# Optimization experiments

Measured on AMD Instinct MI355X. Metric: run time of the kernel, lower is better.

The kernel has to match this reference:

```python
import jax, jax.numpy as jnp
import numpy as np

NUM_HEADS = 16

def setup_inputs() -> dict:
    key = jax.random.key(0)
    ks = jax.random.split(key, 5)
    b, c, w, h = 2, 1024, 48, 48
    sc = 0.02
    return {
        "x": jax.random.normal(ks[0], (b, c, w, h), jnp.float32),
        "Wqkv": jax.random.normal(ks[1], (3 * c, c), jnp.float32) * sc,
        "bqkv": jax.random.normal(ks[2], (3 * c,), jnp.float32) * sc,
        "Wo": jax.random.normal(ks[3], (c, c), jnp.float32) * sc,
        "bo": jax.random.normal(ks[4], (c,), jnp.float32) * sc,
    }

def reference(x, Wqkv, bqkv, Wo, bo):
    b, c, w, h = x.shape
    n = NUM_HEADS
    hd = c // n
    s = w * h
    # [b,c,w,h] -> tokens [b, s, c]
    xs = x.transpose(0, 2, 3, 1).reshape(b, s, c)
    qkv = xs @ Wqkv.T + bqkv                       # [b, s, 3c]
    # rearrange 'b s (three n hd) -> three b n s hd'
    qkv = qkv.reshape(b, s, 3, n, hd).transpose(2, 0, 3, 1, 4)
    q, k, v = qkv[0], qkv[1], qkv[2]               # [b, n, s, hd]
    score = jnp.einsum('bnqh,bnkh->bnqk', q, k) / jnp.sqrt(jnp.float32(hd))
    # module uses a soft causal mask: subtract 10000 above the diagonal
    mask = 10000.0 * jnp.triu(jnp.ones((s, s), dtype=score.dtype), k=1)
    attn = jax.nn.softmax(score - mask, axis=-1)   # [b, n, s, s]
    z = jnp.einsum('bnqk,bnkh->bqnh', attn, v).reshape(b, s, c)
    out = z @ Wo.T + bo                            # [b, s, c]
    return out.reshape(b, w, h, c).transpose(0, 3, 1, 2)
```

## Files before the change

### kernel.cpp

```cpp
#include <hip/hip_runtime.h>

typedef __bf16 bf16;
typedef __bf16 bf16x8 __attribute__((ext_vector_type(8)));
typedef float floatx4 __attribute__((ext_vector_type(4)));

static constexpr int S = 2304;
static constexpr int C = 1024;
static constexpr int NHEAD = 16;
static constexpr int HDIM = 64;
static constexpr int BATCH = 2;

__global__ __launch_bounds__(256) void k_convert(const float* __restrict__ src,
                                                 bf16* __restrict__ dst, int n8) {
  int i = blockIdx.x * 256 + threadIdx.x;
  if (i >= n8) return;
  float4 a = *(const float4*)(src + (size_t)i * 8);
  float4 b = *(const float4*)(src + (size_t)i * 8 + 4);
  bf16x8 o;
  o[0] = (bf16)a.x; o[1] = (bf16)a.y; o[2] = (bf16)a.z; o[3] = (bf16)a.w;
  o[4] = (bf16)b.x; o[5] = (bf16)b.y; o[6] = (bf16)b.z; o[7] = (bf16)b.w;
  *(bf16x8*)(dst + (size_t)i * 8) = o;
}

__global__ __launch_bounds__(256) void k_transpose(const float* __restrict__ x,
                                                   bf16* __restrict__ xs) {
  __shared__ bf16 T[64 * 72];
  int c0 = blockIdx.x * 64, t0 = blockIdx.y * 64, b = blockIdx.z;
  int tid = threadIdx.x;
  const float* xb = x + (size_t)b * C * S;
#pragma unroll
  for (int it = 0; it < 4; ++it) {
    int idx = it * 256 + tid;
    int rc = idx >> 4, t4 = idx & 15;
    float4 v = *(const float4*)(xb + (size_t)(c0 + rc) * S + t0 + t4 * 4);
    T[(t4 * 4 + 0) * 72 + rc] = (bf16)v.x;
    T[(t4 * 4 + 1) * 72 + rc] = (bf16)v.y;
    T[(t4 * 4 + 2) * 72 + rc] = (bf16)v.z;
    T[(t4 * 4 + 3) * 72 + rc] = (bf16)v.w;
  }
  __syncthreads();
  bf16* xsb = xs + (size_t)b * S * C;
#pragma unroll
  for (int it = 0; it < 2; ++it) {
    int idx = it * 256 + tid;
    int rt = idx >> 3, c8 = idx & 7;
    bf16x8 v;
#pragma unroll
    for (int i = 0; i < 8; ++i) v[i] = T[rt * 72 + c8 * 8 + i];
    *(bf16x8*)(xsb + (size_t)(t0 + rt) * C + c0 + c8 * 8) = v;
  }
}

__device__ __forceinline__ void g2l16(const bf16* g, bf16* l) {
  __builtin_amdgcn_global_load_lds(
      (const __attribute__((address_space(1))) void*)g,
      (__attribute__((address_space(3))) void*)l, 16, 0, 0);
}

template <int EPI>
__global__ __launch_bounds__(256) void k_gemm_bt(const bf16* __restrict__ A,
                                                 const bf16* __restrict__ Bt,
                                                 const float* __restrict__ bias,
                                                 bf16* __restrict__ q,
                                                 bf16* __restrict__ k,
                                                 bf16* __restrict__ v,
                                                 float* __restrict__ outf) {
  constexpr int K = C;
  __shared__ bf16 As[128 * 32];
  __shared__ bf16 Bs[128 * 32];
  int tid = threadIdx.x;
  int w = tid >> 6, lane = tid & 63, ln = lane & 15, quad = lane >> 4;
  int m0 = blockIdx.y * 128, n0 = blockIdx.x * 128;
  int moff = (w >> 1) * 64, noff = (w & 1) * 64;
  floatx4 acc[4][4] = {};

  for (int k0 = 0; k0 < K; k0 += 32) {
    __syncthreads();
#pragma unroll
    for (int it = 0; it < 2; ++it) {
      int cb = (it * 4 + w) * 64;
      int g = cb + lane;
      int row = g >> 2, c4 = g & 3;
      g2l16(A + (size_t)(m0 + row) * K + k0 + c4 * 8, As + cb * 8);
      g2l16(Bt + (size_t)(n0 + row) * K + k0 + c4 * 8, Bs + cb * 8);
    }
    __syncthreads();
    bf16x8 af[4], bfr[4];
#pragma unroll
    for (int i = 0; i < 4; ++i) {
      af[i]  = *(const bf16x8*)(As + (moff + i * 16 + ln) * 32 + quad * 8);
      bfr[i] = *(const bf16x8*)(Bs + (noff + i * 16 + ln) * 32 + quad * 8);
    }
#pragma unroll
    for (int im = 0; im < 4; ++im)
#pragma unroll
      for (int in = 0; in < 4; ++in)
        acc[im][in] = __builtin_amdgcn_mfma_f32_16x16x32_bf16(
            af[im], bfr[in], acc[im][in], 0, 0, 0);
  }

  int bidx = (m0 >= S) ? 1 : 0;
  if (EPI == 0) {
#pragma unroll
    for (int in = 0; in < 4; ++in) {
      int j = n0 + noff + in * 16 + ln;
      float bv = bias[j];
      int three = j >> 10;
      int head = (j >> 6) & 15;
      int hdi = j & 63;
#pragma unroll
      for (int im = 0; im < 4; ++im) {
        int mbase = m0 + moff + im * 16 + quad * 4;
        int tb = mbase - bidx * S;
        if (three == 2) {
          union { ushort4 u; bf16 h[4]; } P;
#pragma unroll
          for (int r = 0; r < 4; ++r) P.h[r] = (bf16)(acc[im][in][r] + bv);
          *(ushort4*)(v + ((size_t)(bidx * NHEAD + head) * HDIM + hdi) * S + tb) = P.u;
        } else {
          bf16* dst = (three == 0 ? q : k) +
                      ((size_t)(bidx * NHEAD + head) * S + tb) * HDIM + hdi;
#pragma unroll
          for (int r = 0; r < 4; ++r) dst[(size_t)r * HDIM] = (bf16)(acc[im][in][r] + bv);
        }
      }
    }
  } else {
#pragma unroll
    for (int in = 0; in < 4; ++in) {
      int co = n0 + noff + in * 16 + ln;
      float bv = bias[co];
#pragma unroll
      for (int im = 0; im < 4; ++im) {
        int mbase = m0 + moff + im * 16 + quad * 4;
        int tb = mbase - bidx * S;
        float4 st;
        st.x = acc[im][in][0] + bv;
        st.y = acc[im][in][1] + bv;
        st.z = acc[im][in][2] + bv;
        st.w = acc[im][in][3] + bv;
        *(float4*)(outf + ((size_t)bidx * C + co) * S + tb) = st;
      }
    }
  }
}

__global__ __launch_bounds__(256) void k_attn(const bf16* __restrict__ Qg,
                                              const bf16* __restrict__ Kg,
                                              const bf16* __restrict__ Vtg,
                                              bf16* __restrict__ z) {
  __shared__ bf16 Ks[2][64 * 64];
  __shared__ bf16 Vs[2][64 * 64];
  __shared__ bf16 Pt[64 * 72];
  int i = blockIdx.x;
  int xcd = i & 7, j = i >> 3;
  int grp = j / 36, jq = j % 36;
  int qi = 35 - jq;
  int bh = xcd + 8 * grp;
  int b = bh >> 4, h = bh & 15;
  int tid = threadIdx.x;
  int w = tid >> 6, lane = tid & 63, ln = lane & 15, quad = lane >> 4;
  int q0 = qi * 64;
  int qg = q0 + w * 16 + ln;

  const bf16* kb = Kg + (size_t)bh * S * HDIM;
  const bf16* vb = Vtg + (size_t)bh * HDIM * S;

  int s_row = tid >> 3, s_c8 = tid & 7;
  int s_cs = s_c8 ^ (s_row & 7);
  int s_row2 = (256 + tid) >> 3;
  int s_cs2 = s_c8 ^ (s_row2 & 7);

  const bf16* qb = Qg + ((size_t)bh * S + qg) * HDIM + quad * 8;
  bf16x8 qf0 = *(const bf16x8*)qb;
  bf16x8 qf1 = *(const bf16x8*)(qb + 32);

  float lsum = 0.f;
  floatx4 o_acc[4] = {};

  {
    g2l16(kb + (size_t)s_row * HDIM + s_cs * 8, Ks[0] + tid * 8);
    g2l16(vb + (size_t)s_row * S + s_cs * 8, Vs[0] + tid * 8);
    g2l16(kb + (size_t)s_row2 * HDIM + s_cs2 * 8, Ks[0] + (256 + tid) * 8);
    g2l16(vb + (size_t)s_row2 * S + s_cs2 * 8, Vs[0] + (256 + tid) * 8);
  }

#pragma unroll 1
  for (int kt = 0; kt <= qi; ++kt) {
    int cur = kt & 1;
    __syncthreads();

    if (kt < qi) {
      int nxt = 1 - cur;
      const bf16* kbn = kb + (size_t)(kt + 1) * 64 * HDIM;
      const bf16* vbn = vb + (size_t)(kt + 1) * 64;
      g2l16(kbn + (size_t)s_row * HDIM + s_cs * 8, Ks[nxt] + tid * 8);
      g2l16(vbn + (size_t)s_row * S + s_cs * 8, Vs[nxt] + tid * 8);
      g2l16(kbn + (size_t)s_row2 * HDIM + s_cs2 * 8, Ks[nxt] + (256 + tid) * 8);
      g2l16(vbn + (size_t)s_row2 * S + s_cs2 * 8, Vs[nxt] + (256 + tid) * 8);
    }

    floatx4 s_acc[4] = {};
#pragma unroll
    for (int kf = 0; kf < 4; ++kf) {
      int row = kf * 16 + ln;
      int sw = row & 7;
      bf16x8 k0 = *(const bf16x8*)(Ks[cur] + row * 64 + ((0 ^ sw) ^ quad) * 8);
      s_acc[kf] = __builtin_amdgcn_mfma_f32_16x16x32_bf16(k0, qf0, s_acc[kf], 0, 0, 0);
      bf16x8 k1 = *(const bf16x8*)(Ks[cur] + row * 64 + ((4 ^ sw) ^ quad) * 8);
      s_acc[kf] = __builtin_amdgcn_mfma_f32_16x16x32_bf16(k1, qf1, s_acc[kf], 0, 0, 0);
    }

#pragma unroll
    for (int kf = 0; kf < 4; ++kf) {
      union { ushort4 u; bf16 hh[4]; } P;
#pragma unroll
      for (int r = 0; r < 4; ++r) {
        int kg = kt * 64 + kf * 16 + quad * 4 + r;
        float pv = (kg > qg) ? 0.f : exp2f(s_acc[kf][r] * 0.180336880f);
        lsum += pv;
        P.hh[r] = (bf16)pv;
      }
      *(ushort4*)(Pt + (w * 16 + ln) * 72 + kf * 16 + quad * 4) = P.u;
    }

#pragma unroll
    for (int t = 0; t < 2; ++t) {
      bf16x8 pf = *(const bf16x8*)(Pt + (w * 16 + ln) * 72 + t * 32 + quad * 8);
#pragma unroll
      for (int hf = 0; hf < 4; ++hf) {
        int row = hf * 16 + ln;
        int sw = row & 7;
        bf16x8 vf = *(const bf16x8*)(Vs[cur] + row * 64 + (((t * 4 + quad) ^ sw)) * 8);
        o_acc[hf] = __builtin_amdgcn_mfma_f32_16x16x32_bf16(vf, pf, o_acc[hf], 0, 0, 0);
      }
    }
  }

  lsum += __shfl_xor(lsum, 16);
  lsum += __shfl_xor(lsum, 32);
  float inv = 1.f / lsum;

  bf16* dst = z + ((size_t)b * S + qg) * C + h * HDIM + quad * 4;
#pragma unroll
  for (int hf = 0; hf < 4; ++hf) {
    union { ushort4 u; bf16 hh[4]; } P;
#pragma unroll
    for (int r = 0; r < 4; ++r) P.hh[r] = (bf16)(o_acc[hf][r] * inv);
    *(ushort4*)(dst + hf * 16) = P.u;
  }
}

extern "C" void kernel_launch(void* const* d_in, const int* in_sizes, int n_in,
                              void* d_out, int out_size, void* d_ws, size_t ws_size,
                              hipStream_t stream) {
  const float* x    = (const float*)d_in[0];
  const float* Wqkv = (const float*)d_in[1];
  const float* bqkv = (const float*)d_in[2];
  const float* Wo   = (const float*)d_in[3];
  const float* bo   = (const float*)d_in[4];
  float* out = (float*)d_out;

  bf16* ws = (bf16*)d_ws;
  const size_t tok = (size_t)BATCH * S * C;
  bf16* xs   = ws;
  bf16* Qg   = ws + tok;
  bf16* Kg   = ws + 2 * tok;
  bf16* Vtg  = ws + 3 * tok;
  bf16* Wqb  = ws + 4 * tok;
  bf16* Wob  = Wqb + (size_t)3 * C * C;
  bf16* z    = xs;

  k_convert<<<(3 * C * C / 8 + 255) / 256, 256, 0, stream>>>(Wqkv, Wqb, 3 * C * C / 8);
  k_convert<<<(C * C / 8 + 255) / 256, 256, 0, stream>>>(Wo, Wob, C * C / 8);
  k_transpose<<<dim3(C / 64, S / 64, BATCH), 256, 0, stream>>>(x, xs);
  k_gemm_bt<0><<<dim3(3 * C / 128, BATCH * S / 128), 256, 0, stream>>>(
      xs, Wqb, bqkv, Qg, Kg, Vtg, nullptr);
  k_attn<<<dim3(1152), 256, 0, stream>>>(Qg, Kg, Vtg, z);
  k_gemm_bt<1><<<dim3(C / 128, BATCH * S / 128), 256, 0, stream>>>(
      z, Wob, bo, nullptr, nullptr, nullptr, out);
}
```

Before: 230.7 us.

## Process 128 queries per attention block and fold softmax scale into Q

The attention kernel now handles two 64-row query tiles per block, so each K/V tile loaded into shared memory is reused by both halves and the grid shrinks from 1152 to 576 blocks. The causal mask test is applied only on diagonal tiles, and the fully masked lower-half tile is skipped. The softmax scale (including the log2e factor) is folded into Q in the QKV GEMM epilogue, which removes a multiply per score. In exchange, register pressure goes up, fewer blocks are available to hide latency, and the causal work is less evenly balanced across blocks.

```diff
diff --git a/kernel.cpp b/kernel.cpp
--- a/kernel.cpp
+++ b/kernel.cpp
@@ -9,6 +9,7 @@
 static constexpr int NHEAD = 16;
 static constexpr int HDIM = 64;
 static constexpr int BATCH = 2;
+static constexpr float QSCALE = 0.18033688011112042f;
 
 __global__ __launch_bounds__(256) void k_convert(const float* __restrict__ src,
                                                  bf16* __restrict__ dst, int n8) {
@@ -117,9 +118,13 @@
 #pragma unroll
           for (int r = 0; r < 4; ++r) P.h[r] = (bf16)(acc[im][in][r] + bv);
           *(ushort4*)(v + ((size_t)(bidx * NHEAD + head) * HDIM + hdi) * S + tb) = P.u;
+        } else if (three == 0) {
+          bf16* dst = q + ((size_t)(bidx * NHEAD + head) * S + tb) * HDIM + hdi;
+#pragma unroll
+          for (int r = 0; r < 4; ++r)
+            dst[(size_t)r * HDIM] = (bf16)((acc[im][in][r] + bv) * QSCALE);
         } else {
-          bf16* dst = (three == 0 ? q : k) +
-                      ((size_t)(bidx * NHEAD + head) * S + tb) * HDIM + hdi;
+          bf16* dst = k + ((size_t)(bidx * NHEAD + head) * S + tb) * HDIM + hdi;
 #pragma unroll
           for (int r = 0; r < 4; ++r) dst[(size_t)r * HDIM] = (bf16)(acc[im][in][r] + bv);
         }
@@ -151,103 +156,183 @@
                                               bf16* __restrict__ z) {
   __shared__ bf16 Ks[2][64 * 64];
   __shared__ bf16 Vs[2][64 * 64];
-  __shared__ bf16 Pt[64 * 72];
+  __shared__ bf16 Pt[128 * 72];
   int i = blockIdx.x;
   int xcd = i & 7, j = i >> 3;
-  int grp = j / 36, jq = j % 36;
-  int qi = 35 - jq;
+  int grp = j / 18, jq = j % 18;
+  int qi = 17 - jq;
   int bh = xcd + 8 * grp;
   int b = bh >> 4, h = bh & 15;
   int tid = threadIdx.x;
   int w = tid >> 6, lane = tid & 63, ln = lane & 15, quad = lane >> 4;
-  int q0 = qi * 64;
-  int qg = q0 + w * 16 + ln;
+  int q0 = qi * 128;
+  int qgL = q0 + w * 16 + ln;
+  int qgU = qgL + 64;
 
   const bf16* kb = Kg + (size_t)bh * S * HDIM;
   const bf16* vb = Vtg + (size_t)bh * HDIM * S;
 
   int s_row = tid >> 3, s_c8 = tid & 7;
   int s_cs = s_c8 ^ (s_row & 7);
-  int s_row2 = (256 + tid) >> 3;
+  int s_row2 = s_row + 32;
   int s_cs2 = s_c8 ^ (s_row2 & 7);
-
-  const bf16* qb = Qg + ((size_t)bh * S + qg) * HDIM + quad * 8;
-  bf16x8 qf0 = *(const bf16x8*)qb;
-  bf16x8 qf1 = *(const bf16x8*)(qb + 32);
-
-  float lsum = 0.f;
-  floatx4 o_acc[4] = {};
-
-  {
-    g2l16(kb + (size_t)s_row * HDIM + s_cs * 8, Ks[0] + tid * 8);
-    g2l16(vb + (size_t)s_row * S + s_cs * 8, Vs[0] + tid * 8);
-    g2l16(kb + (size_t)s_row2 * HDIM + s_cs2 * 8, Ks[0] + (256 + tid) * 8);
-    g2l16(vb + (size_t)s_row2 * S + s_cs2 * 8, Vs[0] + (256 + tid) * 8);
-  }
+  size_t kOff1 = (size_t)s_row * HDIM + s_cs * 8;
+  size_t kOff2 = (size_t)s_row2 * HDIM + s_cs2 * 8;
+  size_t vOff1 = (size_t)s_row * S + s_cs * 8;
+  size_t vOff2 = (size_t)s_row2 * S + s_cs2 * 8;
+
+  const bf16* qbL = Qg + ((size_t)bh * S + qgL) * HDIM + quad * 8;
+  const bf16* qbU = qbL + (size_t)64 * HDIM;
+  bf16x8 qfL0 = *(const bf16x8*)qbL;
+  bf16x8 qfL1 = *(const bf16x8*)(qbL + 32);
+  bf16x8 qfU0 = *(const bf16x8*)qbU;
+  bf16x8 qfU1 = *(const bf16x8*)(qbU + 32);
+
+  float lsumL = 0.f, lsumU = 0.f;
+  floatx4 oL[4] = {}, oU[4] = {};
+
+  int ktMax = 2 * qi + 1;
+
+  g2l16(kb + kOff1, Ks[0] + tid * 8);
+  g2l16(vb + vOff1, Vs[0] + tid * 8);
+  g2l16(kb + kOff2, Ks[0] + (256 + tid) * 8);
+  g2l16(vb + vOff2, Vs[0] + (256 + tid) * 8);
+
+  const bf16* kbn = kb + (size_t)64 * HDIM;
+  const bf16* vbn = vb + 64;
 
 #pragma unroll 1
-  for (int kt = 0; kt <= qi; ++kt) {
+  for (int kt = 0; kt <= ktMax; ++kt) {
     int cur = kt & 1;
     __syncthreads();
 
-    if (kt < qi) {
-      int nxt = 1 - cur;
-      const bf16* kbn = kb + (size_t)(kt + 1) * 64 * HDIM;
-      const bf16* vbn = vb + (size_t)(kt + 1) * 64;
-      g2l16(kbn + (size_t)s_row * HDIM + s_cs * 8, Ks[nxt] + tid * 8);
-      g2l16(vbn + (size_t)s_row * S + s_cs * 8, Vs[nxt] + tid * 8);
-      g2l16(kbn + (size_t)s_row2 * HDIM + s_cs2 * 8, Ks[nxt] + (256 + tid) * 8);
-      g2l16(vbn + (size_t)s_row2 * S + s_cs2 * 8, Vs[nxt] + (256 + tid) * 8);
-    }
-
-    floatx4 s_acc[4] = {};
+    if (kt < ktMax) {
+      bf16* kd = Ks[1 - cur];
+      bf16* vd = Vs[1 - cur];
+      g2l16(kbn + kOff1, kd + tid * 8);
+      g2l16(vbn + vOff1, vd + tid * 8);
+      g2l16(kbn + kOff2, kd + (256 + tid) * 8);
+      g2l16(vbn + vOff2, vd + (256 + tid) * 8);
+      kbn += (size_t)64 * HDIM;
+      vbn += 64;
+    }
+
+    bool maskL = (kt == 2 * qi);
+    bool skipL = (kt == 2 * qi + 1);
+    bool maskU = (kt == 2 * qi + 1);
+
+    floatx4 sL[4] = {}, sU[4] = {};
 #pragma unroll
     for (int kf = 0; kf < 4; ++kf) {
       int row = kf * 16 + ln;
       int sw = row & 7;
-      bf16x8 k0 = *(const bf16x8*)(Ks[cur] + row * 64 + ((0 ^ sw) ^ quad) * 8);
-      s_acc[kf] = __builtin_amdgcn_mfma_f32_16x16x32_bf16(k0, qf0, s_acc[kf], 0, 0, 0);
+      bf16x8 k0 = *(const bf16x8*)(Ks[cur] + row * 64 + (sw ^ quad) * 8);
       bf16x8 k1 = *(const bf16x8*)(Ks[cur] + row * 64 + ((4 ^ sw) ^ quad) * 8);
-      s_acc[kf] = __builtin_amdgcn_mfma_f32_16x16x32_bf16(k1, qf1, s_acc[kf], 0, 0, 0);
-    }
-
-#pragma unroll
-    for (int kf = 0; kf < 4; ++kf) {
-      union { ushort4 u; bf16 hh[4]; } P;
-#pragma unroll
-      for (int r = 0; r < 4; ++r) {
-        int kg = kt * 64 + kf * 16 + quad * 4 + r;
-        float pv = (kg > qg) ? 0.f : exp2f(s_acc[kf][r] * 0.180336880f);
-        lsum += pv;
-        P.hh[r] = (bf16)pv;
-      }
-      *(ushort4*)(Pt + (w * 16 + ln) * 72 + kf * 16 + quad * 4) = P.u;
+      sL[kf] = __builtin_amdgcn_mfma_f32_16x16x32_bf16(k0, qfL0, sL[kf], 0, 0, 0);
+      sU[kf] = __builtin_amdgcn_mfma_f32_16x16x32_bf16(k0, qfU0, sU[kf], 0, 0, 0);
+      sL[kf] = __builtin_amdgcn_mfma_f32_16x16x32_bf16(k1, qfL1, sL[kf], 0, 0, 0);
+      sU[kf] = __builtin_amdgcn_mfma_f32_16x16x32_bf16(k1, qfU1, sU[kf], 0, 0, 0);
+    }
+
+    if (!skipL) {
+      if (!maskL) {
+#pragma unroll
+        for (int kf = 0; kf < 4; ++kf) {
+          union { ushort4 u; bf16 hh[4]; } P;
+#pragma unroll
+          for (int r = 0; r < 4; ++r) {
+            float pv = exp2f(sL[kf][r]);
+            lsumL += pv;
+            P.hh[r] = (bf16)pv;
+          }
+          *(ushort4*)(Pt + (w * 16 + ln) * 72 + kf * 16 + quad * 4) = P.u;
+        }
+      } else {
+#pragma unroll
+        for (int kf = 0; kf < 4; ++kf) {
+          union { ushort4 u; bf16 hh[4]; } P;
+#pragma unroll
+          for (int r = 0; r < 4; ++r) {
+            int kg = kt * 64 + kf * 16 + quad * 4 + r;
+            float pv = (kg > qgL) ? 0.f : exp2f(sL[kf][r]);
+            lsumL += pv;
+            P.hh[r] = (bf16)pv;
+          }
+          *(ushort4*)(Pt + (w * 16 + ln) * 72 + kf * 16 + quad * 4) = P.u;
+        }
+      }
+    }
+    if (!maskU) {
+#pragma unroll
+      for (int kf = 0; kf < 4; ++kf) {
+        union { ushort4 u; bf16 hh[4]; } P;
+#pragma unroll
+        for (int r = 0; r < 4; ++r) {
+          float pv = exp2f(sU[kf][r]);
+          lsumU += pv;
+          P.hh[r] = (bf16)pv;
+        }
+        *(ushort4*)(Pt + (64 + w * 16 + ln) * 72 + kf * 16 + quad * 4) = P.u;
+      }
+    } else {
+#pragma unroll
+      for (int kf = 0; kf < 4; ++kf) {
+        union { ushort4 u; bf16 hh[4]; } P;
+#pragma unroll
+        for (int r = 0; r < 4; ++r) {
+          int kg = kt * 64 + kf * 16 + quad * 4 + r;
+          float pv = (kg > qgU) ? 0.f : exp2f(sU[kf][r]);
+          lsumU += pv;
+          P.hh[r] = (bf16)pv;
+        }
+        *(ushort4*)(Pt + (64 + w * 16 + ln) * 72 + kf * 16 + quad * 4) = P.u;
+      }
     }
 
 #pragma unroll
     for (int t = 0; t < 2; ++t) {
-      bf16x8 pf = *(const bf16x8*)(Pt + (w * 16 + ln) * 72 + t * 32 + quad * 8);
-#pragma unroll
-      for (int hf = 0; hf < 4; ++hf) {
-        int row = hf * 16 + ln;
-        int sw = row & 7;
-        bf16x8 vf = *(const bf16x8*)(Vs[cur] + row * 64 + (((t * 4 + quad) ^ sw)) * 8);
-        o_acc[hf] = __builtin_amdgcn_mfma_f32_16x16x32_bf16(vf, pf, o_acc[hf], 0, 0, 0);
-      }
-    }
-  }
-
-  lsum += __shfl_xor(lsum, 16);
-  lsum += __shfl_xor(lsum, 32);
-  float inv = 1.f / lsum;
-
-  bf16* dst = z + ((size_t)b * S + qg) * C + h * HDIM + quad * 4;
+      bf16x8 pfU = *(const bf16x8*)(Pt + (64 + w * 16 + ln) * 72 + t * 32 + quad * 8);
+      if (!skipL) {
+        bf16x8 pfL = *(const bf16x8*)(Pt + (w * 16 + ln) * 72 + t * 32 + quad * 8);
+#pragma unroll
+        for (int hf = 0; hf < 4; ++hf) {
+          int row = hf * 16 + ln;
+          int sw = row & 7;
+          bf16x8 vf = *(const bf16x8*)(Vs[cur] + row * 64 + (((t * 4 + quad) ^ sw)) * 8);
+          oL[hf] = __builtin_amdgcn_mfma_f32_16x16x32_bf16(vf, pfL, oL[hf], 0, 0, 0);
+          oU[hf] = __builtin_amdgcn_mfma_f32_16x16x32_bf16(vf, pfU, oU[hf], 0, 0, 0);
+        }
+      } else {
+#pragma unroll
+        for (int hf = 0; hf < 4; ++hf) {
+          int row = hf * 16 + ln;
+          int sw = row & 7;
+          bf16x8 vf = *(const bf16x8*)(Vs[cur] + row * 64 + (((t * 4 + quad) ^ sw)) * 8);
+          oU[hf] = __builtin_amdgcn_mfma_f32_16x16x32_bf16(vf, pfU, oU[hf], 0, 0, 0);
+        }
+      }
+    }
+  }
+
+  lsumL += __shfl_xor(lsumL, 16);
+  lsumL += __shfl_xor(lsumL, 32);
+  lsumU += __shfl_xor(lsumU, 16);
+  lsumU += __shfl_xor(lsumU, 32);
+  float invL = 1.f / lsumL;
+  float invU = 1.f / lsumU;
+
+  bf16* dstL = z + ((size_t)b * S + qgL) * C + h * HDIM + quad * 4;
+  bf16* dstU = z + ((size_t)b * S + qgU) * C + h * HDIM + quad * 4;
 #pragma unroll
   for (int hf = 0; hf < 4; ++hf) {
-    union { ushort4 u; bf16 hh[4]; } P;
-#pragma unroll
-    for (int r = 0; r < 4; ++r) P.hh[r] = (bf16)(o_acc[hf][r] * inv);
-    *(ushort4*)(dst + hf * 16) = P.u;
+    union { ushort4 u; bf16 hh[4]; } PL, PU;
+#pragma unroll
+    for (int r = 0; r < 4; ++r) {
+      PL.hh[r] = (bf16)(oL[hf][r] * invL);
+      PU.hh[r] = (bf16)(oU[hf][r] * invU);
+    }
+    *(ushort4*)(dstL + hf * 16) = PL.u;
+    *(ushort4*)(dstU + hf * 16) = PU.u;
   }
 }
 
@@ -276,7 +361,7 @@
   k_transpose<<<dim3(C / 64, S / 64, BATCH), 256, 0, stream>>>(x, xs);
   k_gemm_bt<0><<<dim3(3 * C / 128, BATCH * S / 128), 256, 0, stream>>>(
       xs, Wqb, bqkv, Qg, Kg, Vtg, nullptr);
-  k_attn<<<dim3(1152), 256, 0, stream>>>(Qg, Kg, Vtg, z);
+  k_attn<<<dim3(576), 256, 0, stream>>>(Qg, Kg, Vtg, z);
   k_gemm_bt<1><<<dim3(C / 128, BATCH * S / 128), 256, 0, stream>>>(
       z, Wob, bo, nullptr, nullptr, nullptr, out);
 }
```

New measurement: 241.7 us. +4.7%, slower.
